# Performance work log

Measured on AMD Instinct MI355X. Metric: run time of the kernel, lower is better.

Reference implementation:

```python
import jax, jax.numpy as jnp
import numpy as np

N, NCB, DIM, CB_SIZE = 16384, 8, 32, 1024


def setup_inputs() -> dict:
    key = jax.random.key(0)
    k1, k2, k3 = jax.random.split(key, 3)
    x = jax.random.normal(k1, (N, NCB, DIM), dtype=jnp.float32)
    codebook = jax.random.normal(k2, (NCB, CB_SIZE, DIM), dtype=jnp.float32)
    rate_bias = jax.random.normal(k3, (NCB, CB_SIZE), dtype=jnp.float32)
    return {"x": x, "codebook": codebook, "rate_bias": rate_bias}


def reference(x, codebook, rate_bias):
    # x: (N, ncb, dim), codebook: (ncb, cb_size, dim)
    x_sq = jnp.sum(x * x, axis=-1, keepdims=True)            # (N, ncb, 1)
    cb_sq = jnp.sum(codebook * codebook, axis=-1)            # (ncb, cb_size)
    cross = jnp.einsum('nkd,kcd->nkc', x, codebook)          # (N, ncb, cb_size)
    dist = x_sq + cb_sq - 2.0 * cross                        # (N, ncb, cb_size)
    dist = dist + rate_bias                                  # rate_bias broadcast
    index = jnp.argmin(dist, axis=-1, keepdims=True)         # (N, ncb, 1)
    one_hot = jax.nn.one_hot(index[..., 0], CB_SIZE, dtype=dist.dtype)  # (N, ncb, cb_size)
    x_hat = jnp.einsum('nkc,kcd->nkd', one_hot, codebook)    # (N, ncb, dim)
    return (x_hat, one_hot, index)
```

## Files before the change

### kernel.cpp

```cpp
#include <hip/hip_runtime.h>

typedef float f32x4 __attribute__((ext_vector_type(4)));
typedef short bf16x8 __attribute__((ext_vector_type(8)));

#define NN 16384
#define NCB 8
#define DIM 32
#define CB 1024
#define RPB 512
#define EPP 512
#define TPP 32

#define LGK_BARRIER() \
    asm volatile("s_waitcnt lgkmcnt(0)\n\ts_barrier" ::: "memory")

__device__ __forceinline__ unsigned short f2bf(float v) {
    const unsigned u = __float_as_uint(v);
    return (unsigned short)((u + 0x7FFFu + ((u >> 16) & 1u)) >> 16);
}
__device__ __forceinline__ float bf2f(unsigned short s) {
    return __uint_as_float(((unsigned)s) << 16);
}

__device__ __forceinline__ void split3(const f32x4 a, const f32x4 b,
                                       bf16x8* H, bf16x8* M, bf16x8* L) {
    bf16x8 h, m, l;
#pragma unroll
    for (int j = 0; j < 8; ++j) {
        const float vv = (j < 4) ? a[j] : b[j - 4];
        const unsigned short hs = f2bf(vv);
        const float r1 = vv - bf2f(hs);
        const unsigned short ms = f2bf(r1);
        const float r2 = r1 - bf2f(ms);
        h[j] = (short)hs;
        m[j] = (short)ms;
        l[j] = (short)f2bf(r2);
    }
    *H = h;
    *M = m;
    *L = l;
}

__global__ __launch_bounds__(256) void vq_csq(const float* __restrict__ cb,
                                              const float* __restrict__ rb,
                                              float* __restrict__ out) {
    int i = blockIdx.x * 256 + threadIdx.x;
    if (i >= NCB * CB) return;
    const f32x4* c4 = (const f32x4*)(cb + (size_t)i * DIM);
    float s0 = 0.f, s1 = 0.f, s2 = 0.f, s3 = 0.f;
#pragma unroll
    for (int j = 0; j < 8; ++j) {
        f32x4 v = c4[j];
        s0 = fmaf(v[0], v[0], s0);
        s1 = fmaf(v[1], v[1], s1);
        s2 = fmaf(v[2], v[2], s2);
        s3 = fmaf(v[3], v[3], s3);
    }
    out[i] = ((s0 + s1) + (s2 + s3)) + rb[i];
}

__global__ __launch_bounds__(512, 1) void vq_fused(
    const float* __restrict__ x, const float* __restrict__ cb,
    const float* __restrict__ csqb, float* __restrict__ xhat,
    float* __restrict__ onehot, float* __restrict__ idxf) {
    __shared__ short cH[EPP * DIM];
    __shared__ short cM[EPP * DIM];
    __shared__ short cL[EPP * DIM];
    __shared__ float sCq[CB];
    __shared__ unsigned short sIdx[RPB];

    const int tid = threadIdx.x;
    const int w = tid >> 6;
    const int lane = tid & 63;
    const int l15 = lane & 15;
    const int l4 = lane >> 4;
    const int k = blockIdx.x & (NCB - 1);
    const int n0 = (blockIdx.x >> 3) * RPB;

    const float* cbk = cb + (size_t)k * CB * DIM;

    bf16x8 xh[4], xm[4], xl[4];
#pragma unroll
    for (int mt = 0; mt < 4; ++mt) {
        const int row = n0 + w * 64 + mt * 16 + l15;
        const float* xp = x + ((size_t)row * NCB + k) * DIM + l4 * 8;
        split3(*(const f32x4*)xp, *(const f32x4*)(xp + 4), &xh[mt], &xm[mt],
               &xl[mt]);
    }

#pragma unroll
    for (int rd = 0; rd < 4; ++rd) {
        const int eLoc = w * 64 + rd * 16 + l15;
        const float* src = cbk + (size_t)eLoc * DIM + l4 * 8;
        bf16x8 h, m, l;
        split3(*(const f32x4*)src, *(const f32x4*)(src + 4), &h, &m, &l);
        const int so = eLoc * DIM + l4 * 8;
        *(bf16x8*)&cH[so] = h;
        *(bf16x8*)&cM[so] = m;
        *(bf16x8*)&cL[so] = l;
    }
    sCq[tid] = csqb[(size_t)k * CB + tid];
    sCq[tid + 512] = csqb[(size_t)k * CB + tid + 512];
    __syncthreads();

    f32x4 pf[4][2];
#pragma unroll
    for (int rd = 0; rd < 4; ++rd) {
        const int eLoc = w * 64 + rd * 16 + l15;
        const float* src = cbk + (size_t)(EPP + eLoc) * DIM + l4 * 8;
        pf[rd][0] = *(const f32x4*)src;
        pf[rd][1] = *(const f32x4*)(src + 4);
    }

    float best[4][4];
    int bidx[4][4];
#pragma unroll
    for (int mt = 0; mt < 4; ++mt)
#pragma unroll
        for (int r = 0; r < 4; ++r) {
            best[mt][r] = 3.4028235e38f;
            bidx[mt][r] = 0;
        }

    const f32x4 z4 = {0.f, 0.f, 0.f, 0.f};

    for (int p = 0; p < 2; ++p) {
        if (p) {
            LGK_BARRIER();
#pragma unroll
            for (int rd = 0; rd < 4; ++rd) {
                const int eLoc = w * 64 + rd * 16 + l15;
                bf16x8 h, m, l;
                split3(pf[rd][0], pf[rd][1], &h, &m, &l);
                const int so = eLoc * DIM + l4 * 8;
                *(bf16x8*)&cH[so] = h;
                *(bf16x8*)&cM[so] = m;
                *(bf16x8*)&cL[so] = l;
            }
            LGK_BARRIER();
        }

#pragma unroll 2
        for (int tt = 0; tt < TPP; ++tt) {
            {
                f32x4* rp = (f32x4*)onehot +
                            ((size_t)(n0 + w * 64 + p * 32 + tt) * NCB + k) *
                                256;
#pragma unroll
                for (int j = 0; j < 4; ++j) rp[j * 64 + lane] = z4;
            }

            const int so = (tt * 16 + l15) * DIM + l4 * 8;
            const bf16x8 ch = *(const bf16x8*)&cH[so];
            const bf16x8 cm = *(const bf16x8*)&cM[so];
            const bf16x8 cl = *(const bf16x8*)&cL[so];
            const float cqv = sCq[p * EPP + tt * 16 + l15];
            const int eg = p * EPP + tt * 16 + l15;

#pragma unroll
            for (int mt = 0; mt < 4; ++mt) {
                f32x4 acc = {0.f, 0.f, 0.f, 0.f};
                acc = __builtin_amdgcn_mfma_f32_16x16x32_bf16(xh[mt], ch, acc,
                                                              0, 0, 0);
                acc = __builtin_amdgcn_mfma_f32_16x16x32_bf16(xh[mt], cm, acc,
                                                              0, 0, 0);
                acc = __builtin_amdgcn_mfma_f32_16x16x32_bf16(xm[mt], ch, acc,
                                                              0, 0, 0);
                acc = __builtin_amdgcn_mfma_f32_16x16x32_bf16(xm[mt], cm, acc,
                                                              0, 0, 0);
                acc = __builtin_amdgcn_mfma_f32_16x16x32_bf16(xh[mt], cl, acc,
                                                              0, 0, 0);
                acc = __builtin_amdgcn_mfma_f32_16x16x32_bf16(xl[mt], ch, acc,
                                                              0, 0, 0);
#pragma unroll
                for (int r = 0; r < 4; ++r) {
                    const float dist = fmaf(-2.f, acc[r], cqv);
                    if (dist < best[mt][r]) {
                        best[mt][r] = dist;
                        bidx[mt][r] = eg;
                    }
                }
            }
        }
    }

#pragma unroll
    for (int mt = 0; mt < 4; ++mt)
#pragma unroll
        for (int r = 0; r < 4; ++r) {
            float b = best[mt][r];
            int ix = bidx[mt][r];
#pragma unroll
            for (int mask = 1; mask <= 8; mask <<= 1) {
                const float ob = __shfl_xor(b, mask, 64);
                const int oi = __shfl_xor(ix, mask, 64);
                if (ob < b || (ob == b && oi < ix)) {
                    b = ob;
                    ix = oi;
                }
            }
            if (l15 == 0)
                sIdx[w * 64 + mt * 16 + l4 * 4 + r] = (unsigned short)ix;
        }

    const int bx = sIdx[w * 64 + lane];
    const int n = n0 + w * 64 + lane;

    idxf[(size_t)n * NCB + k] = (float)bx;
    const f32x4* srcv = (const f32x4*)(cbk + (size_t)bx * DIM);
    f32x4* dst = (f32x4*)(xhat + ((size_t)n * NCB + k) * DIM);
#pragma unroll
    for (int j = 0; j < 8; ++j) dst[j] = srcv[j];

    asm volatile("s_waitcnt vmcnt(0)" ::: "memory");
    onehot[((size_t)n * NCB + k) * CB + bx] = 1.0f;
}

extern "C" void kernel_launch(void* const* d_in, const int* in_sizes, int n_in,
                              void* d_out, int out_size, void* d_ws,
                              size_t ws_size, hipStream_t stream) {
    const float* x = (const float*)d_in[0];
    const float* cb = (const float*)d_in[1];
    const float* rb = (const float*)d_in[2];

    float* out = (float*)d_out;
    float* xhat = out;
    float* onehot = out + (size_t)NN * NCB * DIM;
    float* idxf = onehot + (size_t)NN * NCB * CB;

    float* csqb = (float*)d_ws;

    vq_csq<<<(NCB * CB + 255) / 256, 256, 0, stream>>>(cb, rb, csqb);
    vq_fused<<<(NN / RPB) * NCB, 512, 0, stream>>>(x, cb, csqb, xhat, onehot,
                                                   idxf);
}
```

Baseline: 150.6 us.

## Move one-hot zero fill into the codebook-norm prelaunch kernel

The 512 MiB one-hot zero fill moves out of the fused MFMA distance loop into the preceding kernel, using 2048 extra blocks alongside the codebook-norm computation. The fused kernel then only scatters the 1.0 entries, so it no longer needs a vmcnt wait between zeroing and the final write. This frees the main loop from interleaved global stores, but the fill is now serialized before the compute kernel instead of overlapping with MFMA work. The custom LDS barriers are also replaced with __syncthreads.

```diff
diff --git a/kernel.cpp b/kernel.cpp
--- a/kernel.cpp
+++ b/kernel.cpp
@@ -10,9 +10,6 @@
 #define RPB 512
 #define EPP 512
 #define TPP 32
-
-#define LGK_BARRIER() \
-    asm volatile("s_waitcnt lgkmcnt(0)\n\ts_barrier" ::: "memory")
 
 __device__ __forceinline__ unsigned short f2bf(float v) {
     const unsigned u = __float_as_uint(v);
@@ -41,10 +38,19 @@
     *L = l;
 }
 
-__global__ __launch_bounds__(256) void vq_csq(const float* __restrict__ cb,
-                                              const float* __restrict__ rb,
-                                              float* __restrict__ out) {
-    int i = blockIdx.x * 256 + threadIdx.x;
+__global__ __launch_bounds__(256) void vq_zero_csq(const float* __restrict__ cb,
+                                                   const float* __restrict__ rb,
+                                                   float* __restrict__ csqb,
+                                                   float* __restrict__ onehot) {
+    const int b = blockIdx.x;
+    if (b < 2048) {
+        f32x4* dst = (f32x4*)onehot + (size_t)b * 16384 + threadIdx.x;
+        const f32x4 z = {0.f, 0.f, 0.f, 0.f};
+#pragma unroll 8
+        for (int i = 0; i < 64; ++i) dst[i * 256] = z;
+        return;
+    }
+    const int i = (b - 2048) * 256 + threadIdx.x;
     if (i >= NCB * CB) return;
     const f32x4* c4 = (const f32x4*)(cb + (size_t)i * DIM);
     float s0 = 0.f, s1 = 0.f, s2 = 0.f, s3 = 0.f;
@@ -56,7 +62,7 @@
         s2 = fmaf(v[2], v[2], s2);
         s3 = fmaf(v[3], v[3], s3);
     }
-    out[i] = ((s0 + s1) + (s2 + s3)) + rb[i];
+    csqb[i] = ((s0 + s1) + (s2 + s3)) + rb[i];
 }
 
 __global__ __launch_bounds__(512, 1) void vq_fused(
@@ -122,11 +128,9 @@
             bidx[mt][r] = 0;
         }
 
-    const f32x4 z4 = {0.f, 0.f, 0.f, 0.f};
-
     for (int p = 0; p < 2; ++p) {
         if (p) {
-            LGK_BARRIER();
+            __syncthreads();
 #pragma unroll
             for (int rd = 0; rd < 4; ++rd) {
                 const int eLoc = w * 64 + rd * 16 + l15;
@@ -137,19 +141,11 @@
                 *(bf16x8*)&cM[so] = m;
                 *(bf16x8*)&cL[so] = l;
             }
-            LGK_BARRIER();
+            __syncthreads();
         }
 
 #pragma unroll 2
         for (int tt = 0; tt < TPP; ++tt) {
-            {
-                f32x4* rp = (f32x4*)onehot +
-                            ((size_t)(n0 + w * 64 + p * 32 + tt) * NCB + k) *
-                                256;
-#pragma unroll
-                for (int j = 0; j < 4; ++j) rp[j * 64 + lane] = z4;
-            }
-
             const int so = (tt * 16 + l15) * DIM + l4 * 8;
             const bf16x8 ch = *(const bf16x8*)&cH[so];
             const bf16x8 cm = *(const bf16x8*)&cM[so];
@@ -207,13 +203,11 @@
     const int n = n0 + w * 64 + lane;
 
     idxf[(size_t)n * NCB + k] = (float)bx;
+    onehot[((size_t)n * NCB + k) * CB + bx] = 1.0f;
     const f32x4* srcv = (const f32x4*)(cbk + (size_t)bx * DIM);
     f32x4* dst = (f32x4*)(xhat + ((size_t)n * NCB + k) * DIM);
 #pragma unroll
     for (int j = 0; j < 8; ++j) dst[j] = srcv[j];
-
-    asm volatile("s_waitcnt vmcnt(0)" ::: "memory");
-    onehot[((size_t)n * NCB + k) * CB + bx] = 1.0f;
 }
 
 extern "C" void kernel_launch(void* const* d_in, const int* in_sizes, int n_in,
@@ -230,7 +224,7 @@
 
     float* csqb = (float*)d_ws;
 
-    vq_csq<<<(NCB * CB + 255) / 256, 256, 0, stream>>>(cb, rb, csqb);
+    vq_zero_csq<<<2048 + 32, 256, 0, stream>>>(cb, rb, csqb, onehot);
     vq_fused<<<(NN / RPB) * NCB, 512, 0, stream>>>(x, cb, csqb, xhat, onehot,
                                                    idxf);
 }
```

Result: slower. 172.0 us (+14.3%).
